# Optimization experiments

Measured on AMD Instinct MI355X. Metric: run time of the kernel, lower is better.

Reference implementation:

```python
import jax, jax.numpy as jnp
import numpy as np

N, M, D, DV = 8192, 8192, 64, 64

def setup_inputs() -> dict:
    key = jax.random.key(0)
    kq, kk, kv = jax.random.split(key, 3)
    Q = jax.random.normal(kq, (N, D), dtype=jnp.float32)
    K = jax.random.normal(kk, (M, D), dtype=jnp.float32)
    V = jax.random.normal(kv, (M, DV), dtype=jnp.float32)
    return {"Q": Q, "K": K, "V": V}

def reference(Q, K, V):
    d = K.shape[-1]
    scores = jnp.einsum('nd,md->nm', Q, K) / jnp.sqrt(jnp.float32(d))  # [N, M]
    attn = jax.nn.softmax(scores, axis=-1)
    return attn @ V  # [N, DV]
```

## Files before the change

### kernel.cpp

```cpp
#include <hip/hip_runtime.h>


#define NQ 8192
#define NK 8192

typedef float f32x4 __attribute__((ext_vector_type(4)));
typedef short short8 __attribute__((ext_vector_type(8)));
union U4 { uint4 u; short8 s; };

#define MFMA16 __builtin_amdgcn_mfma_f32_16x16x32_bf16

__device__ __forceinline__ unsigned pk2(float a, float b) {
    unsigned ua = __builtin_bit_cast(unsigned, a);
    unsigned ub = __builtin_bit_cast(unsigned, b);
    ua = (ua + 0x7FFFu + ((ua >> 16) & 1u)) >> 16;
    ub = (ub + 0x7FFFu + ((ub >> 16) & 1u)) & 0xFFFF0000u;
    return ua | ub;
}

__global__ __launch_bounds__(256)
void prepass(const float* __restrict__ Kg, const float* __restrict__ Vg,
             uint4* __restrict__ Kb4, uint4* __restrict__ Vt4) {
    __shared__ float ld[64 * 33];
    const int t = threadIdx.x, b = blockIdx.x;

    if (b < 256) {
        const int kl = t >> 3, dg = t & 7;
        const int e = kl & 1, i16 = kl >> 1, h = dg >> 2, q = dg & 3;
        const float* gp = Kg + (size_t)(b * 32 + kl) * 64 + dg * 8;
        float4 f0 = *(const float4*)gp;
        float4 f1 = *(const float4*)(gp + 4);
        uint4 o = make_uint4(pk2(f0.x, f0.y), pk2(f0.z, f0.w),
                             pk2(f1.x, f1.y), pk2(f1.z, f1.w));
        Kb4[(size_t)(b * 4 + e * 2 + h) * 64 + i16 * 4 + q] = o;
    } else {
        const int c = b - 256;
        {
            const int key = t >> 3, dg = t & 7;
            const float* gp = Vg + (size_t)(c * 32 + key) * 64 + dg * 8;
            float4 f0 = *(const float4*)gp;
            float4 f1 = *(const float4*)(gp + 4);
            ld[(dg * 8 + 0) * 33 + key] = f0.x;
            ld[(dg * 8 + 1) * 33 + key] = f0.y;
            ld[(dg * 8 + 2) * 33 + key] = f0.z;
            ld[(dg * 8 + 3) * 33 + key] = f0.w;
            ld[(dg * 8 + 4) * 33 + key] = f1.x;
            ld[(dg * 8 + 5) * 33 + key] = f1.y;
            ld[(dg * 8 + 6) * 33 + key] = f1.z;
            ld[(dg * 8 + 7) * 33 + key] = f1.w;
        }
        __syncthreads();
        {
            const int dim = t >> 2, kq = t & 3;
            const int dt = dim >> 4, i16 = dim & 15;
            float v[8];
            #pragma unroll
            for (int j = 0; j < 8; ++j) v[j] = ld[dim * 33 + kq * 8 + j];
            uint4 o = make_uint4(pk2(v[0], v[1]), pk2(v[2], v[3]),
                                 pk2(v[4], v[5]), pk2(v[6], v[7]));
            Vt4[(size_t)(c * 4 + dt) * 64 + i16 * 4 + kq] = o;
        }
    }
}

__global__ __launch_bounds__(512, 1)
void attn_main(const float* __restrict__ Qg,
               const uint4* __restrict__ Kb4,
               const uint4* __restrict__ Vt4,
               float* __restrict__ Og) {
    __shared__ uint4 shb4[2080];
    float* sF = (float*)shb4;
    unsigned* shu = (unsigned*)shb4;

    const int t = threadIdx.x, w = t >> 6, lane = t & 63;
    const int q = lane >> 4, i16 = lane & 15;
    const int qb0 = blockIdx.x * 32;
    const int lsl = i16 * 4 + q;
    const int phase = blockIdx.x & 31;

    const float SCL = 0.18033688011112042f;
    short8 aq0, aq1, aq2, aq3;
    {
        const float* qp0 = Qg + (size_t)(qb0 + i16) * 64 + q * 8;
        const float* qp1 = Qg + (size_t)(qb0 + 16 + i16) * 64 + q * 8;
        U4 u;
        float4 f0, f1;
        f0 = *(const float4*)(qp0);      f1 = *(const float4*)(qp0 + 4);
        u.u = make_uint4(pk2(f0.x * SCL, f0.y * SCL), pk2(f0.z * SCL, f0.w * SCL),
                         pk2(f1.x * SCL, f1.y * SCL), pk2(f1.z * SCL, f1.w * SCL));
        aq0 = u.s;
        f0 = *(const float4*)(qp0 + 32); f1 = *(const float4*)(qp0 + 36);
        u.u = make_uint4(pk2(f0.x * SCL, f0.y * SCL), pk2(f0.z * SCL, f0.w * SCL),
                         pk2(f1.x * SCL, f1.y * SCL), pk2(f1.z * SCL, f1.w * SCL));
        aq1 = u.s;
        f0 = *(const float4*)(qp1);      f1 = *(const float4*)(qp1 + 4);
        u.u = make_uint4(pk2(f0.x * SCL, f0.y * SCL), pk2(f0.z * SCL, f0.w * SCL),
                         pk2(f1.x * SCL, f1.y * SCL), pk2(f1.z * SCL, f1.w * SCL));
        aq2 = u.s;
        f0 = *(const float4*)(qp1 + 32); f1 = *(const float4*)(qp1 + 36);
        u.u = make_uint4(pk2(f0.x * SCL, f0.y * SCL), pk2(f0.z * SCL, f0.w * SCL),
                         pk2(f1.x * SCL, f1.y * SCL), pk2(f1.z * SCL, f1.w * SCL));
        aq3 = u.s;
    }

    f32x4 acc[2][4];
    float lsum[2][4];
    #pragma unroll
    for (int rt = 0; rt < 2; ++rt) {
        #pragma unroll
        for (int dt = 0; dt < 4; ++dt) { acc[rt][dt][0]=0.f; acc[rt][dt][1]=0.f; acc[rt][dt][2]=0.f; acc[rt][dt][3]=0.f; }
        #pragma unroll
        for (int r = 0; r < 4; ++r) lsum[rt][r] = 0.f;
    }

    const int tpw = ((i16 >> 2) & 1) + 2 * q + 32 * (i16 >> 3);
    const int pp  = i16 & 3;
    const int tpr = (q & 1) + 2 * ((i16 >> 2) & 3) + 8 * (i16 & 3) + 32 * (q >> 1);

    uint4 kfA[4], vfA[4], kfB[4], vfB[4], kfC[4], vfC[4];

#define LOAD_T(TT, KD, VD)                                                           \
    do {                                                                             \
        const int cb = ((((TT) + phase) & 31) * 8 + w) * 4;                          \
        _Pragma("unroll")                                                            \
        for (int eh = 0; eh < 4; ++eh)                                               \
            (KD)[eh] = Kb4[(size_t)(cb + eh) * 64 + lsl];                            \
        _Pragma("unroll")                                                            \
        for (int dt = 0; dt < 4; ++dt)                                               \
            (VD)[dt] = Vt4[(size_t)(cb + dt) * 64 + lsl];                            \
    } while (0)

#define COMPUTE(KD, VD)                                                              \
    do {                                                                             \
        U4 ap0, ap1;                                                                 \
        _Pragma("unroll")                                                            \
        for (int rt = 0; rt < 2; ++rt) {                                             \
            f32x4 s0, s1;                                                            \
            s0[0]=-16.f; s0[1]=-16.f; s0[2]=-16.f; s0[3]=-16.f;                      \
            s1[0]=-16.f; s1[1]=-16.f; s1[2]=-16.f; s1[3]=-16.f;                      \
            U4 u0, u1, u2, u3;                                                       \
            u0.u = (KD)[0]; u1.u = (KD)[1]; u2.u = (KD)[2]; u3.u = (KD)[3];          \
            s0 = MFMA16(rt ? aq2 : aq0, u0.s, s0, 0, 0, 0);                          \
            s0 = MFMA16(rt ? aq3 : aq1, u1.s, s0, 0, 0, 0);                          \
            s1 = MFMA16(rt ? aq2 : aq0, u2.s, s1, 0, 0, 0);                          \
            s1 = MFMA16(rt ? aq3 : aq1, u3.s, s1, 0, 0, 0);                          \
            const int rbase = (w * 2 + rt) * 256;                                    \
            _Pragma("unroll")                                                        \
            for (int r = 0; r < 4; ++r) {                                            \
                float p0 = __builtin_amdgcn_exp2f(s0[r]);                            \
                float p1 = __builtin_amdgcn_exp2f(s1[r]);                            \
                lsum[rt][r] += p0;                                                   \
                lsum[rt][r] += p1;                                                   \
                shu[rbase + (tpw + 8 * r) * 4 + pp] = pk2(p0, p1);                   \
            }                                                                        \
        }                                                                            \
        ap0.u = shb4[(w * 2 + 0) * 64 + tpr];                                        \
        ap1.u = shb4[(w * 2 + 1) * 64 + tpr];                                        \
        _Pragma("unroll")                                                            \
        for (int dt = 0; dt < 4; ++dt) {                                             \
            U4 bv; bv.u = (VD)[dt];                                                  \
            acc[0][dt] = MFMA16(ap0.s, bv.s, acc[0][dt], 0, 0, 0);                   \
            acc[1][dt] = MFMA16(ap1.s, bv.s, acc[1][dt], 0, 0, 0);                   \
        }                                                                            \
    } while (0)

    LOAD_T(0, kfA, vfA);
    LOAD_T(1, kfB, vfB);
    LOAD_T(2, kfC, vfC);
    __builtin_amdgcn_sched_barrier(0);
    #pragma unroll 1
    for (int tt = 0; tt < 30; tt += 3) {
        COMPUTE(kfA, vfA);
        LOAD_T(tt + 3, kfA, vfA);
        __builtin_amdgcn_sched_barrier(0);
        COMPUTE(kfB, vfB);
        LOAD_T(tt + 4, kfB, vfB);
        __builtin_amdgcn_sched_barrier(0);
        COMPUTE(kfC, vfC);
        LOAD_T(tt + 5, kfC, vfC);
        __builtin_amdgcn_sched_barrier(0);
    }
    COMPUTE(kfA, vfA);
    COMPUTE(kfB, vfB);

    #pragma unroll
    for (int rt = 0; rt < 2; ++rt)
        #pragma unroll
        for (int r = 0; r < 4; ++r) {
            float v = lsum[rt][r];
            v += __shfl_xor(v, 1);
            v += __shfl_xor(v, 2);
            v += __shfl_xor(v, 4);
            v += __shfl_xor(v, 8);
            lsum[rt][r] = v;
        }

    __syncthreads();
    for (int step = 4; step >= 1; step >>= 1) {
        if (w >= step && w < 2 * step) {
            float* base = sF + (w - step) * 2080;
            #pragma unroll
            for (int rt = 0; rt < 2; ++rt) {
                #pragma unroll
                for (int dt = 0; dt < 4; ++dt)
                    #pragma unroll
                    for (int r = 0; r < 4; ++r)
                        base[(rt * 16 + 4 * q + r) * 64 + dt * 16 + i16] = acc[rt][dt][r];
                if (i16 == 0) {
                    #pragma unroll
                    for (int r = 0; r < 4; ++r) base[2048 + rt * 16 + 4 * q + r] = lsum[rt][r];
                }
            }
        }
        __syncthreads();
        if (w < step) {
            const float* base = sF + w * 2080;
            #pragma unroll
            for (int rt = 0; rt < 2; ++rt) {
                #pragma unroll
                for (int dt = 0; dt < 4; ++dt)
                    #pragma unroll
                    for (int r = 0; r < 4; ++r)
                        acc[rt][dt][r] += base[(rt * 16 + 4 * q + r) * 64 + dt * 16 + i16];
                #pragma unroll
                for (int r = 0; r < 4; ++r) lsum[rt][r] += base[2048 + rt * 16 + 4 * q + r];
            }
        }
        __syncthreads();
    }

    if (w == 0) {
        #pragma unroll
        for (int rt = 0; rt < 2; ++rt)
            #pragma unroll
            for (int r = 0; r < 4; ++r) {
                const float inv = 1.0f / lsum[rt][r];
                #pragma unroll
                for (int dt = 0; dt < 4; ++dt)
                    sF[(rt * 16 + 4 * q + r) * 64 + dt * 16 + i16] = acc[rt][dt][r] * inv;
            }
    }
    __syncthreads();
    {
        const int row = t >> 4, ds = t & 15;
        float4 o = *(const float4*)(sF + row * 64 + ds * 4);
        *(float4*)(Og + (size_t)(qb0 + row) * 64 + ds * 4) = o;
    }
}

extern "C" void kernel_launch(void* const* d_in, const int* in_sizes, int n_in,
                              void* d_out, int out_size, void* d_ws, size_t ws_size,
                              hipStream_t stream) {
    const float* Q = (const float*)d_in[0];
    const float* K = (const float*)d_in[1];
    const float* V = (const float*)d_in[2];
    float* O = (float*)d_out;
    uint4* Kb4 = (uint4*)d_ws;
    uint4* Vt4 = (uint4*)((char*)d_ws + (1 << 20));
    hipLaunchKernelGGL(prepass, dim3(512), dim3(256), 0, stream, K, V, Kb4, Vt4);
    hipLaunchKernelGGL(attn_main, dim3(NQ / 32), dim3(512), 0, stream, Q, Kb4, Vt4, O);
}
```

Before: 97.03 us.

## Split keys across block pairs with 64-row query tiles and merge kernel

Each block now handles 64 query rows instead of 32 and covers only half the key range. Pairs of blocks write unnormalized partial outputs and row sums to workspace, and a third merge kernel adds the halves and normalizes. The goal is to reuse each K/V tile load across twice as many query rows while keeping the same 256-block grid. In exchange it uses more registers per thread (16 accumulators), cuts prefetching from triple to double buffering, and adds partial-result traffic plus an extra launch.

```diff
diff --git a/kernel.cpp b/kernel.cpp
--- a/kernel.cpp
+++ b/kernel.cpp
@@ -67,46 +67,43 @@
 void attn_main(const float* __restrict__ Qg,
                const uint4* __restrict__ Kb4,
                const uint4* __restrict__ Vt4,
-               float* __restrict__ Og) {
-    __shared__ uint4 shb4[2080];
+               float* __restrict__ Opart,
+               float* __restrict__ Lpart) {
+    __shared__ uint4 shb4[4160];
     float* sF = (float*)shb4;
     unsigned* shu = (unsigned*)shb4;
 
     const int t = threadIdx.x, w = t >> 6, lane = t & 63;
     const int q = lane >> 4, i16 = lane & 15;
-    const int qb0 = blockIdx.x * 32;
+    const int bid = blockIdx.x;
+    const int kh = bid & 1;
+    const int rg = bid >> 1;
+    const int qb0 = rg * 64;
     const int lsl = i16 * 4 + q;
-    const int phase = blockIdx.x & 31;
+    const int phase = rg & 15;
 
     const float SCL = 0.18033688011112042f;
-    short8 aq0, aq1, aq2, aq3;
-    {
-        const float* qp0 = Qg + (size_t)(qb0 + i16) * 64 + q * 8;
-        const float* qp1 = Qg + (size_t)(qb0 + 16 + i16) * 64 + q * 8;
+    short8 aq[4][2];
+    #pragma unroll
+    for (int rt = 0; rt < 4; ++rt) {
+        const float* qp = Qg + (size_t)(qb0 + rt * 16 + i16) * 64 + q * 8;
+        float4 f0 = *(const float4*)(qp);
+        float4 f1 = *(const float4*)(qp + 4);
         U4 u;
-        float4 f0, f1;
-        f0 = *(const float4*)(qp0);      f1 = *(const float4*)(qp0 + 4);
         u.u = make_uint4(pk2(f0.x * SCL, f0.y * SCL), pk2(f0.z * SCL, f0.w * SCL),
                          pk2(f1.x * SCL, f1.y * SCL), pk2(f1.z * SCL, f1.w * SCL));
-        aq0 = u.s;
-        f0 = *(const float4*)(qp0 + 32); f1 = *(const float4*)(qp0 + 36);
+        aq[rt][0] = u.s;
+        f0 = *(const float4*)(qp + 32);
+        f1 = *(const float4*)(qp + 36);
         u.u = make_uint4(pk2(f0.x * SCL, f0.y * SCL), pk2(f0.z * SCL, f0.w * SCL),
                          pk2(f1.x * SCL, f1.y * SCL), pk2(f1.z * SCL, f1.w * SCL));
-        aq1 = u.s;
-        f0 = *(const float4*)(qp1);      f1 = *(const float4*)(qp1 + 4);
-        u.u = make_uint4(pk2(f0.x * SCL, f0.y * SCL), pk2(f0.z * SCL, f0.w * SCL),
-                         pk2(f1.x * SCL, f1.y * SCL), pk2(f1.z * SCL, f1.w * SCL));
-        aq2 = u.s;
-        f0 = *(const float4*)(qp1 + 32); f1 = *(const float4*)(qp1 + 36);
-        u.u = make_uint4(pk2(f0.x * SCL, f0.y * SCL), pk2(f0.z * SCL, f0.w * SCL),
-                         pk2(f1.x * SCL, f1.y * SCL), pk2(f1.z * SCL, f1.w * SCL));
-        aq3 = u.s;
-    }
-
-    f32x4 acc[2][4];
-    float lsum[2][4];
+        aq[rt][1] = u.s;
+    }
+
+    f32x4 acc[4][4];
+    float lsum[4][4];
     #pragma unroll
-    for (int rt = 0; rt < 2; ++rt) {
+    for (int rt = 0; rt < 4; ++rt) {
         #pragma unroll
         for (int dt = 0; dt < 4; ++dt) { acc[rt][dt][0]=0.f; acc[rt][dt][1]=0.f; acc[rt][dt][2]=0.f; acc[rt][dt][3]=0.f; }
         #pragma unroll
@@ -117,11 +114,11 @@
     const int pp  = i16 & 3;
     const int tpr = (q & 1) + 2 * ((i16 >> 2) & 3) + 8 * (i16 & 3) + 32 * (q >> 1);
 
-    uint4 kfA[4], vfA[4], kfB[4], vfB[4], kfC[4], vfC[4];
+    uint4 kfA[4], vfA[4], kfB[4], vfB[4];
 
 #define LOAD_T(TT, KD, VD)                                                           \
     do {                                                                             \
-        const int cb = ((((TT) + phase) & 31) * 8 + w) * 4;                          \
+        const int cb = ((kh << 7) + ((((TT) + phase) & 15) * 8 + w)) * 4;            \
         _Pragma("unroll")                                                            \
         for (int eh = 0; eh < 4; ++eh)                                               \
             (KD)[eh] = Kb4[(size_t)(cb + eh) * 64 + lsl];                            \
@@ -132,19 +129,19 @@
 
 #define COMPUTE(KD, VD)                                                              \
     do {                                                                             \
-        U4 ap0, ap1;                                                                 \
-        _Pragma("unroll")                                                            \
-        for (int rt = 0; rt < 2; ++rt) {                                             \
+        U4 ap[4];                                                                    \
+        _Pragma("unroll")                                                            \
+        for (int rt = 0; rt < 4; ++rt) {                                             \
             f32x4 s0, s1;                                                            \
             s0[0]=-16.f; s0[1]=-16.f; s0[2]=-16.f; s0[3]=-16.f;                      \
             s1[0]=-16.f; s1[1]=-16.f; s1[2]=-16.f; s1[3]=-16.f;                      \
             U4 u0, u1, u2, u3;                                                       \
             u0.u = (KD)[0]; u1.u = (KD)[1]; u2.u = (KD)[2]; u3.u = (KD)[3];          \
-            s0 = MFMA16(rt ? aq2 : aq0, u0.s, s0, 0, 0, 0);                          \
-            s0 = MFMA16(rt ? aq3 : aq1, u1.s, s0, 0, 0, 0);                          \
-            s1 = MFMA16(rt ? aq2 : aq0, u2.s, s1, 0, 0, 0);                          \
-            s1 = MFMA16(rt ? aq3 : aq1, u3.s, s1, 0, 0, 0);                          \
-            const int rbase = (w * 2 + rt) * 256;                                    \
+            s0 = MFMA16(aq[rt][0], u0.s, s0, 0, 0, 0);                               \
+            s0 = MFMA16(aq[rt][1], u1.s, s0, 0, 0, 0);                               \
+            s1 = MFMA16(aq[rt][0], u2.s, s1, 0, 0, 0);                               \
+            s1 = MFMA16(aq[rt][1], u3.s, s1, 0, 0, 0);                               \
+            const int rbase = (w * 4 + rt) * 256;                                    \
             _Pragma("unroll")                                                        \
             for (int r = 0; r < 4; ++r) {                                            \
                 float p0 = __builtin_amdgcn_exp2f(s0[r]);                            \
@@ -154,37 +151,31 @@
                 shu[rbase + (tpw + 8 * r) * 4 + pp] = pk2(p0, p1);                   \
             }                                                                        \
         }                                                                            \
-        ap0.u = shb4[(w * 2 + 0) * 64 + tpr];                                        \
-        ap1.u = shb4[(w * 2 + 1) * 64 + tpr];                                        \
+        _Pragma("unroll")                                                            \
+        for (int rt = 0; rt < 4; ++rt) ap[rt].u = shb4[(w * 4 + rt) * 64 + tpr];     \
         _Pragma("unroll")                                                            \
         for (int dt = 0; dt < 4; ++dt) {                                             \
             U4 bv; bv.u = (VD)[dt];                                                  \
-            acc[0][dt] = MFMA16(ap0.s, bv.s, acc[0][dt], 0, 0, 0);                   \
-            acc[1][dt] = MFMA16(ap1.s, bv.s, acc[1][dt], 0, 0, 0);                   \
+            _Pragma("unroll")                                                        \
+            for (int rt = 0; rt < 4; ++rt)                                           \
+                acc[rt][dt] = MFMA16(ap[rt].s, bv.s, acc[rt][dt], 0, 0, 0);          \
         }                                                                            \
     } while (0)
 
     LOAD_T(0, kfA, vfA);
-    LOAD_T(1, kfB, vfB);
-    LOAD_T(2, kfC, vfC);
-    __builtin_amdgcn_sched_barrier(0);
     #pragma unroll 1
-    for (int tt = 0; tt < 30; tt += 3) {
+    for (int tt = 0; tt < 16; tt += 2) {
+        LOAD_T(tt + 1, kfB, vfB);
+        __builtin_amdgcn_sched_barrier(0);
         COMPUTE(kfA, vfA);
-        LOAD_T(tt + 3, kfA, vfA);
+        LOAD_T((tt + 2) & 15, kfA, vfA);
         __builtin_amdgcn_sched_barrier(0);
         COMPUTE(kfB, vfB);
-        LOAD_T(tt + 4, kfB, vfB);
         __builtin_amdgcn_sched_barrier(0);
-        COMPUTE(kfC, vfC);
-        LOAD_T(tt + 5, kfC, vfC);
-        __builtin_amdgcn_sched_barrier(0);
-    }
-    COMPUTE(kfA, vfA);
-    COMPUTE(kfB, vfB);
+    }
 
     #pragma unroll
-    for (int rt = 0; rt < 2; ++rt)
+    for (int rt = 0; rt < 4; ++rt)
         #pragma unroll
         for (int r = 0; r < 4; ++r) {
             float v = lsum[rt][r];
@@ -198,9 +189,9 @@
     __syncthreads();
     for (int step = 4; step >= 1; step >>= 1) {
         if (w >= step && w < 2 * step) {
-            float* base = sF + (w - step) * 2080;
-            #pragma unroll
-            for (int rt = 0; rt < 2; ++rt) {
+            float* base = sF + (w - step) * 4160;
+            #pragma unroll
+            for (int rt = 0; rt < 4; ++rt) {
                 #pragma unroll
                 for (int dt = 0; dt < 4; ++dt)
                     #pragma unroll
@@ -208,22 +199,22 @@
                         base[(rt * 16 + 4 * q + r) * 64 + dt * 16 + i16] = acc[rt][dt][r];
                 if (i16 == 0) {
                     #pragma unroll
-                    for (int r = 0; r < 4; ++r) base[2048 + rt * 16 + 4 * q + r] = lsum[rt][r];
+                    for (int r = 0; r < 4; ++r) base[4096 + rt * 16 + 4 * q + r] = lsum[rt][r];
                 }
             }
         }
         __syncthreads();
         if (w < step) {
-            const float* base = sF + w * 2080;
-            #pragma unroll
-            for (int rt = 0; rt < 2; ++rt) {
+            const float* base = sF + w * 4160;
+            #pragma unroll
+            for (int rt = 0; rt < 4; ++rt) {
                 #pragma unroll
                 for (int dt = 0; dt < 4; ++dt)
                     #pragma unroll
                     for (int r = 0; r < 4; ++r)
                         acc[rt][dt][r] += base[(rt * 16 + 4 * q + r) * 64 + dt * 16 + i16];
                 #pragma unroll
-                for (int r = 0; r < 4; ++r) lsum[rt][r] += base[2048 + rt * 16 + 4 * q + r];
+                for (int r = 0; r < 4; ++r) lsum[rt][r] += base[4096 + rt * 16 + 4 * q + r];
             }
         }
         __syncthreads();
@@ -231,21 +222,37 @@
 
     if (w == 0) {
         #pragma unroll
-        for (int rt = 0; rt < 2; ++rt)
-            #pragma unroll
-            for (int r = 0; r < 4; ++r) {
-                const float inv = 1.0f / lsum[rt][r];
-                #pragma unroll
-                for (int dt = 0; dt < 4; ++dt)
-                    sF[(rt * 16 + 4 * q + r) * 64 + dt * 16 + i16] = acc[rt][dt][r] * inv;
+        for (int rt = 0; rt < 4; ++rt) {
+            #pragma unroll
+            for (int dt = 0; dt < 4; ++dt)
+                #pragma unroll
+                for (int r = 0; r < 4; ++r) {
+                    const int row = qb0 + rt * 16 + 4 * q + r;
+                    Opart[((size_t)kh * 8192 + row) * 64 + dt * 16 + i16] = acc[rt][dt][r];
+                }
+            if (i16 == 0) {
+                #pragma unroll
+                for (int r = 0; r < 4; ++r)
+                    Lpart[kh * 8192 + qb0 + rt * 16 + 4 * q + r] = lsum[rt][r];
             }
-    }
-    __syncthreads();
-    {
-        const int row = t >> 4, ds = t & 15;
-        float4 o = *(const float4*)(sF + row * 64 + ds * 4);
-        *(float4*)(Og + (size_t)(qb0 + row) * 64 + ds * 4) = o;
-    }
+        }
+    }
+}
+
+__global__ __launch_bounds__(256)
+void merge(const float* __restrict__ Opart, const float* __restrict__ Lpart,
+           float* __restrict__ Og) {
+    const int idx = blockIdx.x * 256 + threadIdx.x;
+    const int row = idx >> 4, seg = idx & 15;
+    const float4 a = *(const float4*)(Opart + (size_t)row * 64 + seg * 4);
+    const float4 b = *(const float4*)(Opart + ((size_t)8192 + row) * 64 + seg * 4);
+    const float inv = 1.0f / (Lpart[row] + Lpart[8192 + row]);
+    float4 o;
+    o.x = (a.x + b.x) * inv;
+    o.y = (a.y + b.y) * inv;
+    o.z = (a.z + b.z) * inv;
+    o.w = (a.w + b.w) * inv;
+    *(float4*)(Og + (size_t)row * 64 + seg * 4) = o;
 }
 
 extern "C" void kernel_launch(void* const* d_in, const int* in_sizes, int n_in,
@@ -255,8 +262,12 @@
     const float* K = (const float*)d_in[1];
     const float* V = (const float*)d_in[2];
     float* O = (float*)d_out;
-    uint4* Kb4 = (uint4*)d_ws;
-    uint4* Vt4 = (uint4*)((char*)d_ws + (1 << 20));
+    char* ws = (char*)d_ws;
+    uint4* Kb4   = (uint4*)ws;
+    uint4* Vt4   = (uint4*)(ws + (1 << 20));
+    float* Opart = (float*)(ws + (2 << 20));
+    float* Lpart = (float*)(ws + (6 << 20));
     hipLaunchKernelGGL(prepass, dim3(512), dim3(256), 0, stream, K, V, Kb4, Vt4);
-    hipLaunchKernelGGL(attn_main, dim3(NQ / 32), dim3(512), 0, stream, Q, Kb4, Vt4, O);
-}
+    hipLaunchKernelGGL(attn_main, dim3(256), dim3(512), 0, stream, Q, Kb4, Vt4, Opart, Lpart);
+    hipLaunchKernelGGL(merge, dim3(512), dim3(256), 0, stream, Opart, Lpart, O);
+}
```

Measured after the change: 93.53 us. 1.04x faster.
